# Optimization experiments

Measured on AMD Instinct MI355X. Metric: run time of the kernel, lower is better.

The kernel has to match this reference:

```python
import jax, jax.numpy as jnp
import numpy as np

H = 16
EPS = 1e-6
AUX_COEF = 0.01
TOPK = 2


def _rmsnorm(x, w):
    ms = jnp.mean(x * x, axis=-1, keepdims=True)
    return x * jax.lax.rsqrt(ms + EPS) * w


def _rope(t, cos, sin):
    # t: [B,H,T,hd]; cos/sin: [T, hd//2]
    half = t.shape[-1] // 2
    t1, t2 = t[..., :half], t[..., half:]
    return jnp.concatenate([t1 * cos - t2 * sin, t1 * sin + t2 * cos], axis=-1)


def setup_inputs() -> dict:
    key = jax.random.key(0)
    ks = jax.random.split(key, 16)
    B, T, D = 2, 1024, 1024
    E, I = 8, 4096
    s = lambda k, shp, fan: jax.random.normal(k, shp, dtype=jnp.float32) * (1.0 / np.sqrt(fan))
    return {
        "x": jax.random.normal(ks[0], (B, T, D), dtype=jnp.float32),
        "qkv_w": s(ks[1], (3 * D, D), D),
        "qkv_b": jnp.zeros((3 * D,), jnp.float32),
        "out_w": s(ks[2], (D, D), D),
        "out_b": jnp.zeros((D,), jnp.float32),
        "ln1_w": jnp.ones((D,), jnp.float32),
        "ln2_w": jnp.ones((D,), jnp.float32),
        "gate_w": s(ks[3], (E, D), D),
        "ew1": s(ks[4], (E, I, D), D),
        "eb1": jnp.zeros((E, I), jnp.float32),
        "ew2": s(ks[5], (E, D, I), I),
        "eb2": jnp.zeros((E, D), jnp.float32),
        "ew3": s(ks[6], (E, I, D), D),
        "eb3": jnp.zeros((E, I), jnp.float32),
    }


def _attention(x, qkv_w, qkv_b, out_w, out_b):
    B, T, D = x.shape
    hd = D // H
    half = hd // 2
    qkv = (x @ qkv_w.T + qkv_b).reshape(B, T, H, 3, hd)
    q = jnp.transpose(qkv[..., 0, :], (0, 2, 1, 3))  # [B,H,T,hd]
    k = jnp.transpose(qkv[..., 1, :], (0, 2, 1, 3))
    v = jnp.transpose(qkv[..., 2, :], (0, 2, 1, 3))
    theta = 1.0 / (10000.0 ** (jnp.arange(half, dtype=jnp.float32) / half))
    freq = jnp.arange(T, dtype=jnp.float32)[:, None] * theta[None, :]  # [T,half]
    cos, sin = jnp.cos(freq), jnp.sin(freq)
    q = _rope(q, cos, sin)
    k = _rope(k, cos, sin)
    # NOTE: original scales by embed_dim**-0.5 (not head_dim**-0.5)
    scale = D ** (-0.5)
    scores = jnp.einsum("bhqd,bhkd->bhqk", q, k) * scale
    mask = jnp.triu(jnp.full((T, T), -1e9, dtype=scores.dtype), k=1)
    w = jax.nn.softmax(scores + mask, axis=-1)
    attn = jnp.einsum("bhqk,bhkd->bhqd", w, v)
    attn = jnp.transpose(attn, (0, 2, 1, 3)).reshape(B, T, D)
    return attn @ out_w.T + out_b


def _moe(x, gate_w, ew1, eb1, ew2, eb2, ew3, eb3):
    B, T, D = x.shape
    E = gate_w.shape[0]
    xf = x.reshape(-1, D)  # [N,D]
    N = xf.shape[0]
    probs = jax.nn.softmax(xf @ gate_w.T, axis=-1)  # [N,E]
    topk_vals, topk_idx = jax.lax.top_k(probs, TOPK)
    oh = jax.nn.one_hot(topk_idx, E, dtype=xf.dtype)  # [N,K,E]
    gates = jnp.sum(oh * topk_vals[..., None], axis=1)  # [N,E] dense gate, zero off top-k
    # per-expert SwiGLU over all tokens, combined with sparse gates
    h = jax.nn.silu(jnp.einsum("nd,eid->nei", xf, ew1) + eb1) * (
        jnp.einsum("nd,eid->nei", xf, ew3) + eb3
    )  # [N,E,I]
    out_e = jnp.einsum("nei,edi->ned", h, ew2) + eb2  # [N,E,D]
    y = jnp.einsum("ned,ne->nd", out_e, gates)
    counts = jnp.sum(oh, axis=(0, 1))  # bincount of routed assignments
    f = counts / (N * TOPK)
    P = jnp.mean(probs, axis=0)
    aux = AUX_COEF * E * jnp.dot(f, P)
    return y.reshape(B, T, D), aux


def reference(x, qkv_w, qkv_b, out_w, out_b, ln1_w, ln2_w, gate_w, ew1, eb1, ew2, eb2, ew3, eb3):
    h1 = x + _attention(_rmsnorm(x, ln1_w), qkv_w, qkv_b, out_w, out_b)
    y, aux = _moe(_rmsnorm(h1, ln2_w), gate_w, ew1, eb1, ew2, eb2, ew3, eb3)
    return h1 + y, aux
```

## Files before the change

kernel.cpp:

```cpp
#include <hip/hip_runtime.h>
#include <cstdint>
#include <cstddef>
#include <math.h>

#define T_SEQ  1024
#define DMODEL 1024
#define NHEAD  16
#define HDIM   64
#define NEXP   8
#define IDIM   4096
#define NTOK   2048
#define NSLOT  4096

typedef short bf16x8 __attribute__((ext_vector_type(8)));
typedef short s16x4  __attribute__((ext_vector_type(4)));
typedef float floatx4 __attribute__((ext_vector_type(4)));
typedef unsigned int uintx4 __attribute__((ext_vector_type(4)));

__device__ __forceinline__ float bf2f(short s) {
  return __uint_as_float(((unsigned)(unsigned short)s) << 16);
}
__device__ __forceinline__ short f2bf(float f) {
  unsigned u = __float_as_uint(f);
  unsigned r = (u + 0x7FFFu + ((u >> 16) & 1u)) >> 16;
  return (short)r;
}
__device__ __forceinline__ unsigned cvt_pk_bf16(float lo, float hi) {
  unsigned r;
  asm("v_cvt_pk_bf16_f32 %0, %1, %2" : "=v"(r) : "v"(lo), "v"(hi));
  return r;
}
__device__ __forceinline__ uintx4 pack8_bf16(floatx4 a, floatx4 b) {
  uintx4 u;
  u[0] = cvt_pk_bf16(a[0], a[1]);
  u[1] = cvt_pk_bf16(a[2], a[3]);
  u[2] = cvt_pk_bf16(b[0], b[1]);
  u[3] = cvt_pk_bf16(b[2], b[3]);
  return u;
}
__device__ __forceinline__ void split8(const float* x, uintx4& hi, uintx4& lo) {
  #pragma unroll
  for (int i = 0; i < 4; i++) {
    unsigned h = cvt_pk_bf16(x[2*i], x[2*i+1]);
    hi[i] = h;
    float r0 = x[2*i]   - __uint_as_float(h << 16);
    float r1 = x[2*i+1] - __uint_as_float(h & 0xffff0000u);
    lo[i] = cvt_pk_bf16(r0, r1);
  }
}

__global__ __launch_bounds__(256) void rmsnorm_f32_kernel(
    const float* __restrict__ x, const float* __restrict__ w, float* __restrict__ out) {
  int row = blockIdx.x, tid = threadIdx.x;
  const floatx4* xr = (const floatx4*)(x + (size_t)row * DMODEL);
  floatx4 v = xr[tid];
  float ss = v[0]*v[0] + v[1]*v[1] + v[2]*v[2] + v[3]*v[3];
  #pragma unroll
  for (int off = 32; off > 0; off >>= 1) ss += __shfl_xor(ss, off);
  __shared__ float wsum[4];
  int wid = tid >> 6;
  if ((tid & 63) == 0) wsum[wid] = ss;
  __syncthreads();
  float tot = wsum[0] + wsum[1] + wsum[2] + wsum[3];
  float r = rsqrtf(tot * (1.0f / DMODEL) + 1e-6f);
  floatx4 wv = ((const floatx4*)w)[tid];
  floatx4 o;
  o[0] = v[0]*r*wv[0]; o[1] = v[1]*r*wv[1];
  o[2] = v[2]*r*wv[2]; o[3] = v[3]*r*wv[3];
  ((floatx4*)(out + (size_t)row * DMODEL))[tid] = o;
}

__global__ __launch_bounds__(256) void rmsnorm_bf16_kernel(
    const float* __restrict__ x, const float* __restrict__ w, short* __restrict__ out) {
  int row = blockIdx.x, tid = threadIdx.x;
  const floatx4* xr = (const floatx4*)(x + (size_t)row * DMODEL);
  floatx4 v = xr[tid];
  float ss = v[0]*v[0] + v[1]*v[1] + v[2]*v[2] + v[3]*v[3];
  #pragma unroll
  for (int off = 32; off > 0; off >>= 1) ss += __shfl_xor(ss, off);
  __shared__ float wsum[4];
  int wid = tid >> 6;
  if ((tid & 63) == 0) wsum[wid] = ss;
  __syncthreads();
  float tot = wsum[0] + wsum[1] + wsum[2] + wsum[3];
  float r = rsqrtf(tot * (1.0f / DMODEL) + 1e-6f);
  floatx4 wv = ((const floatx4*)w)[tid];
  s16x4 o;
  o[0] = f2bf(v[0]*r*wv[0]); o[1] = f2bf(v[1]*r*wv[1]);
  o[2] = f2bf(v[2]*r*wv[2]); o[3] = f2bf(v[3]*r*wv[3]);
  *(s16x4*)(out + (size_t)row * DMODEL + tid*4) = o;
}

template<int RESID>
__global__ __launch_bounds__(256) void gemm_3bf16(
    const float* __restrict__ A, const float* __restrict__ W,
    const float* __restrict__ bias, const float* __restrict__ resid,
    float* __restrict__ C, int N, int K) {
  __shared__ __attribute__((aligned(16))) short Ahi[64*40];
  __shared__ __attribute__((aligned(16))) short Alo[64*40];
  __shared__ __attribute__((aligned(16))) short Whi[64*40];
  __shared__ __attribute__((aligned(16))) short Wlo[64*40];
  int tid = threadIdx.x, lane = tid & 63, wid = tid >> 6;
  int wm = wid >> 1, wn = wid & 1;
  int m0 = blockIdx.y * 64, n0 = blockIdx.x * 64;
  floatx4 zero4 = {0.f,0.f,0.f,0.f};
  floatx4 acc[2][2];
  #pragma unroll
  for (int mi = 0; mi < 2; mi++)
    #pragma unroll
    for (int nj = 0; nj < 2; nj++) acc[mi][nj] = zero4;

  int ar = tid >> 2, ak = (tid & 3) * 8;
  const float* Ap = A + (size_t)(m0 + ar) * K + ak;
  const float* Wp = W + (size_t)(n0 + ar) * K + ak;
  int rsel = lane & 15, kseg = (lane >> 4) * 8;

  for (int kk = 0; kk < K; kk += 32) {
    float abuf[8], wbuf[8];
    *(floatx4*)(abuf)     = *(const floatx4*)(Ap + kk);
    *(floatx4*)(abuf + 4) = *(const floatx4*)(Ap + kk + 4);
    *(floatx4*)(wbuf)     = *(const floatx4*)(Wp + kk);
    *(floatx4*)(wbuf + 4) = *(const floatx4*)(Wp + kk + 4);
    uintx4 ahi, alo, whi, wlo;
    split8(abuf, ahi, alo);
    split8(wbuf, whi, wlo);
    __syncthreads();
    *(uintx4*)(&Ahi[ar*40 + ak]) = ahi;
    *(uintx4*)(&Alo[ar*40 + ak]) = alo;
    *(uintx4*)(&Whi[ar*40 + ak]) = whi;
    *(uintx4*)(&Wlo[ar*40 + ak]) = wlo;
    __syncthreads();
    bf16x8 afh[2], afl[2], wfh[2], wfl[2];
    #pragma unroll
    for (int mi = 0; mi < 2; mi++) {
      int row = (wm*32 + mi*16 + rsel)*40 + kseg;
      afh[mi] = *(const bf16x8*)(&Ahi[row]);
      afl[mi] = *(const bf16x8*)(&Alo[row]);
    }
    #pragma unroll
    for (int nj = 0; nj < 2; nj++) {
      int row = (wn*32 + nj*16 + rsel)*40 + kseg;
      wfh[nj] = *(const bf16x8*)(&Whi[row]);
      wfl[nj] = *(const bf16x8*)(&Wlo[row]);
    }
    #pragma unroll
    for (int mi = 0; mi < 2; mi++)
      #pragma unroll
      for (int nj = 0; nj < 2; nj++) {
        acc[mi][nj] = __builtin_amdgcn_mfma_f32_16x16x32_bf16(afl[mi], wfh[nj], acc[mi][nj], 0, 0, 0);
        acc[mi][nj] = __builtin_amdgcn_mfma_f32_16x16x32_bf16(afh[mi], wfl[nj], acc[mi][nj], 0, 0, 0);
        acc[mi][nj] = __builtin_amdgcn_mfma_f32_16x16x32_bf16(afh[mi], wfh[nj], acc[mi][nj], 0, 0, 0);
      }
  }
  int rj = (lane >> 4) * 4, cn = lane & 15;
  #pragma unroll
  for (int mi = 0; mi < 2; mi++) {
    #pragma unroll
    for (int nj = 0; nj < 2; nj++) {
      int n = n0 + wn*32 + nj*16 + cn;
      float bn = bias[n];
      #pragma unroll
      for (int j = 0; j < 4; j++) {
        int m = m0 + wm*32 + mi*16 + rj + j;
        float v = acc[mi][nj][j] + bn;
        if (RESID) v += resid[(size_t)m * N + n];
        C[(size_t)m * N + n] = v;
      }
    }
  }
}

__global__ void rope_table_kernel(float* __restrict__ cost, float* __restrict__ sint) {
  int t = blockIdx.x, d = threadIdx.x;
  double theta = pow(10000.0, -(double)d / 32.0);
  double f = (double)t * theta;
  cost[t*32 + d] = (float)cos(f);
  sint[t*32 + d] = (float)sin(f);
}

__global__ __launch_bounds__(256) void rope_kernel(
    const float* __restrict__ qkv, const float* __restrict__ cost, const float* __restrict__ sint,
    float* __restrict__ qr, float* __restrict__ kr) {
  int wid = threadIdx.x >> 6, lane = threadIdx.x & 63;
  int idx = blockIdx.x * 4 + wid;
  int h = idx & 15, n = idx >> 4;
  int t = n & (T_SEQ - 1), b = n >> 10;
  const float* base = qkv + (size_t)n * 3072 + h * 192;
  int d2 = lane & 31;
  float c = cost[t*32 + d2], s = sint[t*32 + d2];
  float q1 = base[d2],      q2 = base[d2 + 32];
  float k1 = base[64 + d2], k2 = base[96 + d2];
  float qo = (lane < 32) ? (q1*c - q2*s) : (q1*s + q2*c);
  float ko = (lane < 32) ? (k1*c - k2*s) : (k1*s + k2*c);
  size_t orow = ((size_t)(b*NHEAD + h) * T_SEQ + t) * HDIM;
  qr[orow + lane] = qo;
  kr[orow + lane] = ko;
}

__global__ __launch_bounds__(256) void vtrans_kernel(
    const float* __restrict__ qkvf, float* __restrict__ vrT) {
  __shared__ __attribute__((aligned(16))) float tile[64][68];
  int bh = blockIdx.x, t0 = blockIdx.y * 64;
  int b = bh >> 4, h = bh & 15;
  int tid = threadIdx.x;
  int r = tid >> 2, seg = (tid & 3) * 16;
  const float* src = qkvf + ((size_t)(b*T_SEQ + t0 + r))*3072 + h*192 + 128 + seg;
  floatx4 v0 = *(const floatx4*)(src);
  floatx4 v1 = *(const floatx4*)(src + 4);
  floatx4 v2 = *(const floatx4*)(src + 8);
  floatx4 v3 = *(const floatx4*)(src + 12);
  *(floatx4*)(&tile[r][seg])      = v0;
  *(floatx4*)(&tile[r][seg + 4])  = v1;
  *(floatx4*)(&tile[r][seg + 8])  = v2;
  *(floatx4*)(&tile[r][seg + 12]) = v3;
  __syncthreads();
  int dr = r, tseg = seg;
  floatx4 o0, o1, o2, o3;
  #pragma unroll
  for (int i = 0; i < 4; i++) {
    o0[i] = tile[tseg + i][dr];
    o1[i] = tile[tseg + 4 + i][dr];
    o2[i] = tile[tseg + 8 + i][dr];
    o3[i] = tile[tseg + 12 + i][dr];
  }
  float* dst = vrT + ((size_t)(bh*HDIM + dr))*T_SEQ + t0 + tseg;
  *(floatx4*)(dst)      = o0;
  *(floatx4*)(dst + 4)  = o1;
  *(floatx4*)(dst + 8)  = o2;
  *(floatx4*)(dst + 12) = o3;
}

__global__ __launch_bounds__(256) void attn_mfma_kernel(
    const float* __restrict__ qr_, const float* __restrict__ kr_,
    const float* __restrict__ vrT_, float* __restrict__ attno) {
  __shared__ __attribute__((aligned(16))) short Qhi[64*72];
  __shared__ __attribute__((aligned(16))) short Qlo[64*72];
  __shared__ __attribute__((aligned(16))) short Khi[64*72];
  __shared__ __attribute__((aligned(16))) short Klo[64*72];
  __shared__ __attribute__((aligned(16))) short Vhi[64*72];
  __shared__ __attribute__((aligned(16))) short Vlo[64*72];
  __shared__ __attribute__((aligned(16))) unsigned Pp[64*68];
  int tid = threadIdx.x, lane = tid & 63, w = tid >> 6;
  int bh = blockIdx.x;
  int qt = 15 - (int)blockIdx.y;
  int q0 = qt * 64;
  int b = bh >> 4, h = bh & 15;
  const float* Qb  = qr_  + ((size_t)bh * T_SEQ + q0) * HDIM;
  const float* Kb  = kr_  + (size_t)bh * T_SEQ * HDIM;
  const float* Vtb = vrT_ + (size_t)bh * HDIM * T_SEQ;

  int srow = tid >> 2, sseg = (tid & 3) * 16;
  {
    const float* src = Qb + srow*HDIM + sseg;
    float b0[8], b1[8];
    *(floatx4*)(b0)   = *(const floatx4*)(src);
    *(floatx4*)(b0+4) = *(const floatx4*)(src + 4);
    *(floatx4*)(b1)   = *(const floatx4*)(src + 8);
    *(floatx4*)(b1+4) = *(const floatx4*)(src + 12);
    uintx4 h0, l0, h1, l1;
    split8(b0, h0, l0); split8(b1, h1, l1);
    *(uintx4*)(&Qhi[srow*72 + sseg])     = h0;
    *(uintx4*)(&Qhi[srow*72 + sseg + 8]) = h1;
    *(uintx4*)(&Qlo[srow*72 + sseg])     = l0;
    *(uintx4*)(&Qlo[srow*72 + sseg + 8]) = l1;
  }

  int rsel = lane & 15, kseg = (lane >> 4) * 8, cl = lane & 15;
  int rbase = w*16 + (lane >> 4) * 4;
  const float scale = 0.03125f;
  float mrow[4] = {-1e30f,-1e30f,-1e30f,-1e30f};
  float lrow[4] = {0.f,0.f,0.f,0.f};
  floatx4 zero4 = {0.f,0.f,0.f,0.f};
  floatx4 Of[4];
  #pragma unroll
  for (int f = 0; f < 4; f++) Of[f] = zero4;

  int ntiles = qt + 1;
  for (int kt = 0; kt < ntiles; kt++) {
    int kbase = kt << 6;
    const float* kp = Kb  + (size_t)(kbase + srow)*HDIM + sseg;
    const float* vp = Vtb + (size_t)srow*T_SEQ + kbase + sseg;
    float kb0[8], kb1[8], vb0[8], vb1[8];
    *(floatx4*)(kb0)   = *(const floatx4*)(kp);
    *(floatx4*)(kb0+4) = *(const floatx4*)(kp + 4);
    *(floatx4*)(kb1)   = *(const floatx4*)(kp + 8);
    *(floatx4*)(kb1+4) = *(const floatx4*)(kp + 12);
    *(floatx4*)(vb0)   = *(const floatx4*)(vp);
    *(floatx4*)(vb0+4) = *(const floatx4*)(vp + 4);
    *(floatx4*)(vb1)   = *(const floatx4*)(vp + 8);
    *(floatx4*)(vb1+4) = *(const floatx4*)(vp + 12);
    __syncthreads();
    {
      uintx4 h0, l0, h1, l1;
      split8(kb0, h0, l0); split8(kb1, h1, l1);
      *(uintx4*)(&Khi[srow*72 + sseg])     = h0;
      *(uintx4*)(&Khi[srow*72 + sseg + 8]) = h1;
      *(uintx4*)(&Klo[srow*72 + sseg])     = l0;
      *(uintx4*)(&Klo[srow*72 + sseg + 8]) = l1;
      split8(vb0, h0, l0); split8(vb1, h1, l1);
      *(uintx4*)(&Vhi[srow*72 + sseg])     = h0;
      *(uintx4*)(&Vhi[srow*72 + sseg + 8]) = h1;
      *(uintx4*)(&Vlo[srow*72 + sseg])     = l0;
      *(uintx4*)(&Vlo[srow*72 + sseg + 8]) = l1;
    }
    __syncthreads();
    floatx4 sf[4];
    #pragma unroll
    for (int f = 0; f < 4; f++) sf[f] = zero4;
    #pragma unroll
    for (int c = 0; c < 2; c++) {
      int ko = c*32 + kseg;
      bf16x8 qh = *(const bf16x8*)(&Qhi[(w*16 + rsel)*72 + ko]);
      bf16x8 ql = *(const bf16x8*)(&Qlo[(w*16 + rsel)*72 + ko]);
      #pragma unroll
      for (int f = 0; f < 4; f++) {
        bf16x8 kh = *(const bf16x8*)(&Khi[(f*16 + rsel)*72 + ko]);
        bf16x8 kl = *(const bf16x8*)(&Klo[(f*16 + rsel)*72 + ko]);
        sf[f] = __builtin_amdgcn_mfma_f32_16x16x32_bf16(ql, kh, sf[f], 0, 0, 0);
        sf[f] = __builtin_amdgcn_mfma_f32_16x16x32_bf16(qh, kl, sf[f], 0, 0, 0);
        sf[f] = __builtin_amdgcn_mfma_f32_16x16x32_bf16(qh, kh, sf[f], 0, 0, 0);
      }
    }
    float pm[4] = {-1e30f,-1e30f,-1e30f,-1e30f};
    #pragma unroll
    for (int f = 0; f < 4; f++) {
      int col = kbase + f*16 + cl;
      #pragma unroll
      for (int j = 0; j < 4; j++) {
        float s = sf[f][j];
        s = (col <= q0 + rbase + j) ? s*scale : -1e30f;
        sf[f][j] = s;
        pm[j] = fmaxf(pm[j], s);
      }
    }
    #pragma unroll
    for (int off = 1; off < 16; off <<= 1)
      #pragma unroll
      for (int j = 0; j < 4; j++) pm[j] = fmaxf(pm[j], __shfl_xor(pm[j], off));
    float sc[4], rs[4] = {0.f,0.f,0.f,0.f};
    #pragma unroll
    for (int j = 0; j < 4; j++) {
      float mn = fmaxf(mrow[j], pm[j]);
      sc[j] = __expf(mrow[j] - mn);
      mrow[j] = mn;
    }
    #pragma unroll
    for (int f = 0; f < 4; f++) {
      #pragma unroll
      for (int j = 0; j < 4; j++) {
        float p = (sf[f][j] > -1e29f) ? __expf(sf[f][j] - mrow[j]) : 0.f;
        rs[j] += p;
        unsigned hp = cvt_pk_bf16(p, 0.f);
        float ph = __uint_as_float(hp << 16);
        unsigned lp = cvt_pk_bf16(p - ph, 0.f);
        Pp[(rbase + j)*68 + f*16 + cl] = (hp << 16) | (lp & 0xffffu);
      }
    }
    #pragma unroll
    for (int off = 1; off < 16; off <<= 1)
      #pragma unroll
      for (int j = 0; j < 4; j++) rs[j] += __shfl_xor(rs[j], off);
    #pragma unroll
    for (int j = 0; j < 4; j++) lrow[j] = lrow[j]*sc[j] + rs[j];
    #pragma unroll
    for (int f = 0; f < 4; f++)
      #pragma unroll
      for (int j = 0; j < 4; j++) Of[f][j] *= sc[j];
    __syncthreads();
    #pragma unroll
    for (int c = 0; c < 2; c++) {
      int prow = (w*16 + rsel)*68 + c*32 + kseg;
      uintx4 d0 = *(const uintx4*)(&Pp[prow]);
      uintx4 d1 = *(const uintx4*)(&Pp[prow + 4]);
      uintx4 phw, plw;
      phw[0] = (d0[0] >> 16) | (d0[1] & 0xffff0000u);
      phw[1] = (d0[2] >> 16) | (d0[3] & 0xffff0000u);
      phw[2] = (d1[0] >> 16) | (d1[1] & 0xffff0000u);
      phw[3] = (d1[2] >> 16) | (d1[3] & 0xffff0000u);
      plw[0] = (d0[0] & 0xffffu) | (d0[1] << 16);
      plw[1] = (d0[2] & 0xffffu) | (d0[3] << 16);
      plw[2] = (d1[0] & 0xffffu) | (d1[1] << 16);
      plw[3] = (d1[2] & 0xffffu) | (d1[3] << 16);
      bf16x8 Ph = *(bf16x8*)&phw;
      bf16x8 Pl = *(bf16x8*)&plw;
      int ko = c*32 + kseg;
      #pragma unroll
      for (int f = 0; f < 4; f++) {
        bf16x8 vh = *(const bf16x8*)(&Vhi[(f*16 + rsel)*72 + ko]);
        bf16x8 vl = *(const bf16x8*)(&Vlo[(f*16 + rsel)*72 + ko]);
        Of[f] = __builtin_amdgcn_mfma_f32_16x16x32_bf16(Pl, vh, Of[f], 0, 0, 0);
        Of[f] = __builtin_amdgcn_mfma_f32_16x16x32_bf16(Ph, vl, Of[f], 0, 0, 0);
        Of[f] = __builtin_amdgcn_mfma_f32_16x16x32_bf16(Ph, vh, Of[f], 0, 0, 0);
      }
    }
  }
  #pragma unroll
  for (int j = 0; j < 4; j++) {
    float inv = 1.0f / lrow[j];
    size_t rowoff = ((size_t)(b*T_SEQ + q0 + rbase + j))*DMODEL + h*HDIM;
    #pragma unroll
    for (int f = 0; f < 4; f++)
      attno[rowoff + f*16 + cl] = Of[f][j] * inv;
  }
}

__global__ __launch_bounds__(64) void gate_kernel(
    const float* __restrict__ h1, const float* __restrict__ lnw, const float* __restrict__ gw,
    float* __restrict__ probs, int* __restrict__ pair, float* __restrict__ gpair,
    int* __restrict__ counts) {
  int n = blockIdx.x, lane = threadIdx.x;
  const float* xp = h1 + (size_t)n * DMODEL + lane*16;
  float xv[16];
  double ss = 0.0;
  #pragma unroll
  for (int j = 0; j < 16; j++) { xv[j] = xp[j]; ss += (double)xv[j] * (double)xv[j]; }
  #pragma unroll
  for (int off = 32; off > 0; off >>= 1) ss += __shfl_xor(ss, off);
  double r = 1.0 / sqrt(ss * (1.0 / DMODEL) + 1e-6);
  const float* wp = lnw + lane*16;
  double xf[16];
  #pragma unroll
  for (int j = 0; j < 16; j++) xf[j] = (double)xv[j] * r * (double)wp[j];
  double logit[8];
  #pragma unroll
  for (int e = 0; e < 8; e++) {
    const float* g = gw + e*DMODEL + lane*16;
    double acc = 0.0;
    #pragma unroll
    for (int j = 0; j < 16; j++) acc += xf[j] * (double)g[j];
    logit[e] = acc;
  }
  #pragma unroll
  for (int e = 0; e < 8; e++)
    #pragma unroll
    for (int off = 32; off > 0; off >>= 1) logit[e] += __shfl_xor(logit[e], off);
  double mxl = logit[0];
  #pragma unroll
  for (int e = 1; e < 8; e++) mxl = fmax(mxl, logit[e]);
  double p[8], Z = 0.0;
  #pragma unroll
  for (int e = 0; e < 8; e++) { p[e] = exp(logit[e] - mxl); Z += p[e]; }
  double invZ = 1.0 / Z;
  #pragma unroll
  for (int e = 0; e < 8; e++) p[e] *= invZ;
  int e0 = 0; double b0 = p[0];
  #pragma unroll
  for (int e = 1; e < 8; e++) if (p[e] > b0) { b0 = p[e]; e0 = e; }
  int e1 = -1; double b1 = -1.0;
  #pragma unroll
  for (int e = 0; e < 8; e++) if (e != e0 && p[e] > b1) { b1 = p[e]; e1 = e; }
  if (lane == 0) {
    #pragma unroll
    for (int e = 0; e < 8; e++) probs[n*8 + e] = (float)p[e];
    pair[2*n] = e0; pair[2*n+1] = e1;
    gpair[2*n] = (float)b0; gpair[2*n+1] = (float)b1;
    atomicAdd(&counts[e0], 1);
    atomicAdd(&counts[e1], 1);
  }
}

__global__ void offsets_kernel(const int* __restrict__ counts, int* __restrict__ off,
                               int* __restrict__ cursor) {
  if (threadIdx.x == 0) {
    int a = 0;
    for (int e = 0; e < 8; e++) { off[e] = a; cursor[e] = a; a += counts[e]; }
    off[8] = a;
  }
}

__global__ __launch_bounds__(256) void scatter_kernel(
    const int* __restrict__ pair, const float* __restrict__ gpair, int* __restrict__ cursor,
    int* __restrict__ tok_of_slot, float* __restrict__ gate_of_slot, int* __restrict__ slot_of_tok) {
  int n = blockIdx.x * 256 + threadIdx.x;
  int e0 = pair[2*n], e1 = pair[2*n+1];
  int s0 = atomicAdd(&cursor[e0], 1);
  tok_of_slot[s0] = n; gate_of_slot[s0] = gpair[2*n];   slot_of_tok[2*n] = s0;
  int s1 = atomicAdd(&cursor[e1], 1);
  tok_of_slot[s1] = n; gate_of_slot[s1] = gpair[2*n+1]; slot_of_tok[2*n+1] = s1;
}

__global__ __launch_bounds__(256) void aux_kernel(
    const float* __restrict__ probs, const int* __restrict__ counts, float* __restrict__ outaux) {
  __shared__ double sm[256];
  int t = threadIdx.x;
  int e = t & 7, base = t >> 3;
  double acc = 0.0;
  for (int n = base; n < NTOK; n += 32) acc += (double)probs[n*8 + e];
  sm[t] = acc;
  __syncthreads();
  if (t < 8) {
    double s = 0.0;
    for (int g = 0; g < 32; g++) s += sm[g*8 + t];
    sm[t] = s;
  }
  __syncthreads();
  if (t == 0) {
    double aux = 0.0;
    for (int ee = 0; ee < 8; ee++)
      aux += ((double)counts[ee] * (1.0 / (NTOK*2))) * (sm[ee] * (1.0 / NTOK));
    outaux[0] = (float)(0.08 * aux);
  }
}

__global__ __launch_bounds__(256) void moe13_kernel(
    const short* __restrict__ xn2,
    const float* __restrict__ ew1, const float* __restrict__ eb1,
    const float* __restrict__ ew3, const float* __restrict__ eb3,
    const int* __restrict__ counts, const int* __restrict__ off,
    const int* __restrict__ tok_of_slot, short* __restrict__ hbuf) {
  int e = blockIdx.z;
  int Me = counts[e];
  int m0 = blockIdx.y * 128;
  if (m0 >= Me) return;
  int base = off[e];
  int i0 = blockIdx.x * 64;
  __shared__ __attribute__((aligned(16))) short As[128*40];
  __shared__ __attribute__((aligned(16))) short W1s[64*40];
  __shared__ __attribute__((aligned(16))) short W3s[64*40];
  int tid = threadIdx.x, lane = tid & 63, wid = tid >> 6;
  int wm = wid >> 1, wn = wid & 1;
  floatx4 zero4 = {0.f,0.f,0.f,0.f};
  floatx4 acc1[4][2], acc3[4][2];
  #pragma unroll
  for (int mi = 0; mi < 4; mi++)
    #pragma unroll
    for (int nj = 0; nj < 2; nj++) { acc1[mi][nj] = zero4; acc3[mi][nj] = zero4; }

  int ar = tid >> 1, ak = (tid & 1) * 8;
  int am = m0 + ar;
  bool aval = (am < Me);
  const short* Ag = xn2 + (size_t)(aval ? tok_of_slot[base + am] : 0) * DMODEL;
  int wr = tid >> 2, wk = (tid & 3) * 8;
  const float* W1g = ew1 + ((size_t)e*IDIM + i0 + wr)*DMODEL + wk;
  const float* W3g = ew3 + ((size_t)e*IDIM + i0 + wr)*DMODEL + wk;
  int rsel = lane & 15, kseg = (lane >> 4) * 8;

  for (int kk = 0; kk < DMODEL; kk += 32) {
    bf16x8 a0 = {0,0,0,0,0,0,0,0}, a1 = {0,0,0,0,0,0,0,0};
    if (aval) {
      a0 = *(const bf16x8*)(Ag + kk + ak);
      a1 = *(const bf16x8*)(Ag + kk + ak + 16);
    }
    floatx4 u0 = *(const floatx4*)(W1g + kk);
    floatx4 u1 = *(const floatx4*)(W1g + kk + 4);
    floatx4 v0 = *(const floatx4*)(W3g + kk);
    floatx4 v1 = *(const floatx4*)(W3g + kk + 4);
    __syncthreads();
    *(bf16x8*)(&As[ar*40 + ak])      = a0;
    *(bf16x8*)(&As[ar*40 + ak + 16]) = a1;
    *(uintx4*)(&W1s[wr*40 + wk]) = pack8_bf16(u0, u1);
    *(uintx4*)(&W3s[wr*40 + wk]) = pack8_bf16(v0, v1);
    __syncthreads();
    bf16x8 af[4], w1f[2], w3f[2];
    #pragma unroll
    for (int mi = 0; mi < 4; mi++)
      af[mi] = *(const bf16x8*)(&As[(wm*64 + mi*16 + rsel)*40 + kseg]);
    #pragma unroll
    for (int nj = 0; nj < 2; nj++) {
      w1f[nj] = *(const bf16x8*)(&W1s[(wn*32 + nj*16 + rsel)*40 + kseg]);
      w3f[nj] = *(const bf16x8*)(&W3s[(wn*32 + nj*16 + rsel)*40 + kseg]);
    }
    #pragma unroll
    for (int mi = 0; mi < 4; mi++)
      #pragma unroll
      for (int nj = 0; nj < 2; nj++) {
        acc1[mi][nj] = __builtin_amdgcn_mfma_f32_16x16x32_bf16(af[mi], w1f[nj], acc1[mi][nj], 0, 0, 0);
        acc3[mi][nj] = __builtin_amdgcn_mfma_f32_16x16x32_bf16(af[mi], w3f[nj], acc3[mi][nj], 0, 0, 0);
      }
  }
  int rj = (lane >> 4) * 4, cn = lane & 15;
  #pragma unroll
  for (int mi = 0; mi < 4; mi++) {
    #pragma unroll
    for (int nj = 0; nj < 2; nj++) {
      int i = i0 + wn*32 + nj*16 + cn;
      float be1 = eb1[e*IDIM + i], be3 = eb3[e*IDIM + i];
      #pragma unroll
      for (int j = 0; j < 4; j++) {
        int m = m0 + wm*64 + mi*16 + rj + j;
        if (m < Me) {
          float a = acc1[mi][nj][j] + be1;
          float b = acc3[mi][nj][j] + be3;
          float hval = (a / (1.f + __expf(-a))) * b;
          hbuf[(size_t)(base + m)*IDIM + i] = f2bf(hval);
        }
      }
    }
  }
}

__global__ __launch_bounds__(256) void moe2_kernel(
    const short* __restrict__ hbuf, const float* __restrict__ ew2, const float* __restrict__ eb2,
    const int* __restrict__ counts, const int* __restrict__ off,
    const float* __restrict__ gate_of_slot,
    float* __restrict__ y0, float* __restrict__ y1) {
  int e = blockIdx.z;
  int Me = counts[e];
  int m0 = blockIdx.y * 128;
  if (m0 >= Me) return;
  int base = off[e];
  int n0 = (blockIdx.x & 7) * 128;
  int khalf = blockIdx.x >> 3;
  int kbeg = khalf * (IDIM/2);
  __shared__ __attribute__((aligned(16))) short As[128*40];
  __shared__ __attribute__((aligned(16))) short Ws[128*40];
  int tid = threadIdx.x, lane = tid & 63, wid = tid >> 6;
  int wm = wid >> 1, wn = wid & 1;
  floatx4 zero4 = {0.f,0.f,0.f,0.f};
  floatx4 acc[4][4];
  #pragma unroll
  for (int mi = 0; mi < 4; mi++)
    #pragma unroll
    for (int nj = 0; nj < 4; nj++) acc[mi][nj] = zero4;

  int ar = tid >> 1, ak = (tid & 1) * 8, kw = (tid & 1) * 16;
  bool aval = (m0 + ar) < Me;
  const short* Ag = hbuf + (size_t)(base + (aval ? (m0 + ar) : 0)) * IDIM + kbeg;
  const float* Wg = ew2 + ((size_t)e*DMODEL + n0 + ar)*IDIM + kbeg;
  int rsel = lane & 15, kseg = (lane >> 4) * 8;

  for (int kk = 0; kk < IDIM/2; kk += 32) {
    bf16x8 a0 = {0,0,0,0,0,0,0,0}, a1 = {0,0,0,0,0,0,0,0};
    if (aval) {
      a0 = *(const bf16x8*)(Ag + kk + ak);
      a1 = *(const bf16x8*)(Ag + kk + ak + 16);
    }
    floatx4 w0 = *(const floatx4*)(Wg + kk + kw);
    floatx4 w1 = *(const floatx4*)(Wg + kk + kw + 4);
    floatx4 w2 = *(const floatx4*)(Wg + kk + kw + 8);
    floatx4 w3 = *(const floatx4*)(Wg + kk + kw + 12);
    __syncthreads();
    *(bf16x8*)(&As[ar*40 + ak])      = a0;
    *(bf16x8*)(&As[ar*40 + ak + 16]) = a1;
    *(uintx4*)(&Ws[ar*40 + kw])     = pack8_bf16(w0, w1);
    *(uintx4*)(&Ws[ar*40 + kw + 8]) = pack8_bf16(w2, w3);
    __syncthreads();
    bf16x8 af[4], wf[4];
    #pragma unroll
    for (int mi = 0; mi < 4; mi++)
      af[mi] = *(const bf16x8*)(&As[(wm*64 + mi*16 + rsel)*40 + kseg]);
    #pragma unroll
    for (int nj = 0; nj < 4; nj++)
      wf[nj] = *(const bf16x8*)(&Ws[(wn*64 + nj*16 + rsel)*40 + kseg]);
    #pragma unroll
    for (int mi = 0; mi < 4; mi++)
      #pragma unroll
      for (int nj = 0; nj < 4; nj++)
        acc[mi][nj] = __builtin_amdgcn_mfma_f32_16x16x32_bf16(af[mi], wf[nj], acc[mi][nj], 0, 0, 0);
  }
  int rj = (lane >> 4) * 4, cn = lane & 15;
  float* yout = khalf ? y1 : y0;
  #pragma unroll
  for (int mi = 0; mi < 4; mi++) {
    #pragma unroll
    for (int nj = 0; nj < 4; nj++) {
      int n = n0 + wn*64 + nj*16 + cn;
      float bn = khalf ? 0.f : eb2[e*DMODEL + n];
      #pragma unroll
      for (int j = 0; j < 4; j++) {
        int m = m0 + wm*64 + mi*16 + rj + j;
        if (m < Me) {
          float g = gate_of_slot[base + m];
          yout[(size_t)(base + m)*DMODEL + n] = (acc[mi][nj][j] + bn) * g;
        }
      }
    }
  }
}

__global__ __launch_bounds__(256) void combine_kernel(
    const float* __restrict__ h1, const float* __restrict__ y0, const float* __restrict__ y1,
    const int* __restrict__ slot_of_tok, float* __restrict__ out) {
  int n = blockIdx.x, t = threadIdx.x;
  int sA = slot_of_tok[2*n], sB = slot_of_tok[2*n+1];
  const floatx4* a   = (const floatx4*)(h1 + (size_t)n*DMODEL);
  const floatx4* y0a = (const floatx4*)(y0 + (size_t)sA*DMODEL);
  const floatx4* y1a = (const floatx4*)(y1 + (size_t)sA*DMODEL);
  const floatx4* y0b = (const floatx4*)(y0 + (size_t)sB*DMODEL);
  const floatx4* y1b = (const floatx4*)(y1 + (size_t)sB*DMODEL);
  floatx4 v = a[t] + (y0a[t] + y1a[t]) + (y0b[t] + y1b[t]);
  ((floatx4*)(out + (size_t)n*DMODEL))[t] = v;
}

extern "C" void kernel_launch(void* const* d_in, const int* in_sizes, int n_in,
                              void* d_out, int out_size, void* d_ws, size_t ws_size,
                              hipStream_t stream) {
  const float* x      = (const float*)d_in[0];
  const float* qkv_w  = (const float*)d_in[1];
  const float* qkv_b  = (const float*)d_in[2];
  const float* out_w  = (const float*)d_in[3];
  const float* out_b  = (const float*)d_in[4];
  const float* ln1_w  = (const float*)d_in[5];
  const float* ln2_w  = (const float*)d_in[6];
  const float* gate_w = (const float*)d_in[7];
  const float* ew1    = (const float*)d_in[8];
  const float* eb1    = (const float*)d_in[9];
  const float* ew2    = (const float*)d_in[10];
  const float* eb2    = (const float*)d_in[11];
  const float* ew3    = (const float*)d_in[12];
  const float* eb3    = (const float*)d_in[13];
  float* out = (float*)d_out;

  char* ws = (char*)d_ws;
  float* xn1f   = (float*)(ws + 0);
  float* attnof = (float*)(ws + 0);
  float* qkvf   = (float*)(ws + 8388608);
  float* h1     = (float*)(ws + 8388608);
  short* xn2    = (short*)(ws + 16777216);
  float* yslot1 = (float*)(ws + 16777216);
  float* qrf    = (float*)(ws + 33554432);
  float* krf    = (float*)(ws + 41943040);
  float* vrT    = (float*)(ws + 50331648);
  short* hbuf   = (short*)(ws + 33554432);
  float* yslot0 = (float*)(ws + 67108864);
  float* cost         = (float*)(ws + 83886080);
  float* sint         = (float*)(ws + 84017152);
  float* probs        = (float*)(ws + 84148224);
  int*   ctrl         = (int*)  (ws + 84213760);
  int*   pair         = (int*)  (ws + 84214784);
  float* gpair        = (float*)(ws + 84231168);
  int*   slot_of_tok  = (int*)  (ws + 84247552);
  int*   tok_of_slot  = (int*)  (ws + 84263936);
  float* gate_of_slot = (float*)(ws + 84280320);

  int* counts = ctrl;
  int* off    = ctrl + 8;
  int* cursor = ctrl + 20;

  hipMemsetAsync(ctrl, 0, 1024, stream);
  rope_table_kernel<<<T_SEQ, 32, 0, stream>>>(cost, sint);
  rmsnorm_f32_kernel<<<NTOK, 256, 0, stream>>>(x, ln1_w, xn1f);
  gemm_3bf16<0><<<dim3(48, 32), 256, 0, stream>>>(xn1f, qkv_w, qkv_b, nullptr, qkvf, 3072, DMODEL);
  rope_kernel<<<8192, 256, 0, stream>>>(qkvf, cost, sint, qrf, krf);
  vtrans_kernel<<<dim3(32, 16), 256, 0, stream>>>(qkvf, vrT);
  attn_mfma_kernel<<<dim3(32, 16), 256, 0, stream>>>(qrf, krf, vrT, attnof);
  gemm_3bf16<1><<<dim3(16, 32), 256, 0, stream>>>(attnof, out_w, out_b, x, h1, DMODEL, DMODEL);
  rmsnorm_bf16_kernel<<<NTOK, 256, 0, stream>>>(h1, ln2_w, xn2);
  gate_kernel<<<NTOK, 64, 0, stream>>>(h1, ln2_w, gate_w, probs, pair, gpair, counts);
  offsets_kernel<<<1, 64, 0, stream>>>(counts, off, cursor);
  scatter_kernel<<<8, 256, 0, stream>>>(pair, gpair, cursor, tok_of_slot, gate_of_slot, slot_of_tok);
  aux_kernel<<<1, 256, 0, stream>>>(probs, counts, out + 2097152);
  moe13_kernel<<<dim3(64, 16, 8), 256, 0, stream>>>(xn2, ew1, eb1, ew3, eb3, counts, off, tok_of_slot, hbuf);
  moe2_kernel<<<dim3(16, 16, 8), 256, 0, stream>>>(hbuf, ew2, eb2, counts, off, gate_of_slot, yslot0, yslot1);
  combine_kernel<<<NTOK, 256, 0, stream>>>(h1, yslot0, yslot1, slot_of_tok, out);
}
```

Before: 545.2 us.

## Load MoE GEMM operands directly from global memory, dropping LDS staging

```diff
diff --git a/kernel.cpp b/kernel.cpp
--- a/kernel.cpp
+++ b/kernel.cpp
@@ -514,11 +514,10 @@
   if (m0 >= Me) return;
   int base = off[e];
   int i0 = blockIdx.x * 64;
-  __shared__ __attribute__((aligned(16))) short As[128*40];
-  __shared__ __attribute__((aligned(16))) short W1s[64*40];
-  __shared__ __attribute__((aligned(16))) short W3s[64*40];
   int tid = threadIdx.x, lane = tid & 63, wid = tid >> 6;
   int wm = wid >> 1, wn = wid & 1;
+  int rsel = lane & 15, kseg = (lane >> 4) * 8;
+
   floatx4 zero4 = {0.f,0.f,0.f,0.f};
   floatx4 acc1[4][2], acc3[4][2];
   #pragma unroll
@@ -526,39 +525,37 @@
     #pragma unroll
     for (int nj = 0; nj < 2; nj++) { acc1[mi][nj] = zero4; acc3[mi][nj] = zero4; }
 
-  int ar = tid >> 1, ak = (tid & 1) * 8;
-  int am = m0 + ar;
-  bool aval = (am < Me);
-  const short* Ag = xn2 + (size_t)(aval ? tok_of_slot[base + am] : 0) * DMODEL;
-  int wr = tid >> 2, wk = (tid & 3) * 8;
-  const float* W1g = ew1 + ((size_t)e*IDIM + i0 + wr)*DMODEL + wk;
-  const float* W3g = ew3 + ((size_t)e*IDIM + i0 + wr)*DMODEL + wk;
-  int rsel = lane & 15, kseg = (lane >> 4) * 8;
+  const short* aptr[4];
+  #pragma unroll
+  for (int mi = 0; mi < 4; mi++) {
+    int m = m0 + wm*64 + mi*16 + rsel;
+    int tok = (m < Me) ? tok_of_slot[base + m] : 0;
+    aptr[mi] = xn2 + (size_t)tok * DMODEL + kseg;
+  }
+  const float* w1p[2];
+  const float* w3p[2];
+  #pragma unroll
+  for (int nj = 0; nj < 2; nj++) {
+    int i = i0 + wn*32 + nj*16 + rsel;
+    w1p[nj] = ew1 + ((size_t)e*IDIM + i)*DMODEL + kseg;
+    w3p[nj] = ew3 + ((size_t)e*IDIM + i)*DMODEL + kseg;
+  }
 
   for (int kk = 0; kk < DMODEL; kk += 32) {
-    bf16x8 a0 = {0,0,0,0,0,0,0,0}, a1 = {0,0,0,0,0,0,0,0};
-    if (aval) {
-      a0 = *(const bf16x8*)(Ag + kk + ak);
-      a1 = *(const bf16x8*)(Ag + kk + ak + 16);
-    }
-    floatx4 u0 = *(const floatx4*)(W1g + kk);
-    floatx4 u1 = *(const floatx4*)(W1g + kk + 4);
-    floatx4 v0 = *(const floatx4*)(W3g + kk);
-    floatx4 v1 = *(const floatx4*)(W3g + kk + 4);
-    __syncthreads();
-    *(bf16x8*)(&As[ar*40 + ak])      = a0;
-    *(bf16x8*)(&As[ar*40 + ak + 16]) = a1;
-    *(uintx4*)(&W1s[wr*40 + wk]) = pack8_bf16(u0, u1);
-    *(uintx4*)(&W3s[wr*40 + wk]) = pack8_bf16(v0, v1);
-    __syncthreads();
     bf16x8 af[4], w1f[2], w3f[2];
     #pragma unroll
     for (int mi = 0; mi < 4; mi++)
-      af[mi] = *(const bf16x8*)(&As[(wm*64 + mi*16 + rsel)*40 + kseg]);
+      af[mi] = *(const bf16x8*)(aptr[mi] + kk);
     #pragma unroll
     for (int nj = 0; nj < 2; nj++) {
-      w1f[nj] = *(const bf16x8*)(&W1s[(wn*32 + nj*16 + rsel)*40 + kseg]);
-      w3f[nj] = *(const bf16x8*)(&W3s[(wn*32 + nj*16 + rsel)*40 + kseg]);
+      floatx4 u0 = *(const floatx4*)(w1p[nj] + kk);
+      floatx4 u1 = *(const floatx4*)(w1p[nj] + kk + 4);
+      uintx4 pw = pack8_bf16(u0, u1);
+      w1f[nj] = *(bf16x8*)&pw;
+      floatx4 v0 = *(const floatx4*)(w3p[nj] + kk);
+      floatx4 v1 = *(const floatx4*)(w3p[nj] + kk + 4);
+      uintx4 pv = pack8_bf16(v0, v1);
+      w3f[nj] = *(bf16x8*)&pv;
     }
     #pragma unroll
     for (int mi = 0; mi < 4; mi++)
@@ -602,10 +599,10 @@
   int n0 = (blockIdx.x & 7) * 128;
   int khalf = blockIdx.x >> 3;
   int kbeg = khalf * (IDIM/2);
-  __shared__ __attribute__((aligned(16))) short As[128*40];
-  __shared__ __attribute__((aligned(16))) short Ws[128*40];
   int tid = threadIdx.x, lane = tid & 63, wid = tid >> 6;
   int wm = wid >> 1, wn = wid & 1;
+  int rsel = lane & 15, kseg = (lane >> 4) * 8;
+
   floatx4 zero4 = {0.f,0.f,0.f,0.f};
   floatx4 acc[4][4];
   #pragma unroll
@@ -613,35 +610,32 @@
     #pragma unroll
     for (int nj = 0; nj < 4; nj++) acc[mi][nj] = zero4;
 
-  int ar = tid >> 1, ak = (tid & 1) * 8, kw = (tid & 1) * 16;
-  bool aval = (m0 + ar) < Me;
-  const short* Ag = hbuf + (size_t)(base + (aval ? (m0 + ar) : 0)) * IDIM + kbeg;
-  const float* Wg = ew2 + ((size_t)e*DMODEL + n0 + ar)*IDIM + kbeg;
-  int rsel = lane & 15, kseg = (lane >> 4) * 8;
+  const short* aptr[4];
+  #pragma unroll
+  for (int mi = 0; mi < 4; mi++) {
+    int m = m0 + wm*64 + mi*16 + rsel;
+    int row = base + ((m < Me) ? m : 0);
+    aptr[mi] = hbuf + (size_t)row*IDIM + kbeg + kseg;
+  }
+  const float* wp[4];
+  #pragma unroll
+  for (int nj = 0; nj < 4; nj++) {
+    int n = n0 + wn*64 + nj*16 + rsel;
+    wp[nj] = ew2 + ((size_t)e*DMODEL + n)*IDIM + kbeg + kseg;
+  }
 
   for (int kk = 0; kk < IDIM/2; kk += 32) {
-    bf16x8 a0 = {0,0,0,0,0,0,0,0}, a1 = {0,0,0,0,0,0,0,0};
-    if (aval) {
-      a0 = *(const bf16x8*)(Ag + kk + ak);
-      a1 = *(const bf16x8*)(Ag + kk + ak + 16);
-    }
-    floatx4 w0 = *(const floatx4*)(Wg + kk + kw);
-    floatx4 w1 = *(const floatx4*)(Wg + kk + kw + 4);
-    floatx4 w2 = *(const floatx4*)(Wg + kk + kw + 8);
-    floatx4 w3 = *(const floatx4*)(Wg + kk + kw + 12);
-    __syncthreads();
-    *(bf16x8*)(&As[ar*40 + ak])      = a0;
-    *(bf16x8*)(&As[ar*40 + ak + 16]) = a1;
-    *(uintx4*)(&Ws[ar*40 + kw])     = pack8_bf16(w0, w1);
-    *(uintx4*)(&Ws[ar*40 + kw + 8]) = pack8_bf16(w2, w3);
-    __syncthreads();
     bf16x8 af[4], wf[4];
     #pragma unroll
     for (int mi = 0; mi < 4; mi++)
-      af[mi] = *(const bf16x8*)(&As[(wm*64 + mi*16 + rsel)*40 + kseg]);
-    #pragma unroll
-    for (int nj = 0; nj < 4; nj++)
-      wf[nj] = *(const bf16x8*)(&Ws[(wn*64 + nj*16 + rsel)*40 + kseg]);
+      af[mi] = *(const bf16x8*)(aptr[mi] + kk);
+    #pragma unroll
+    for (int nj = 0; nj < 4; nj++) {
+      floatx4 u0 = *(const floatx4*)(wp[nj] + kk);
+      floatx4 u1 = *(const floatx4*)(wp[nj] + kk + 4);
+      uintx4 pw = pack8_bf16(u0, u1);
+      wf[nj] = *(bf16x8*)&pw;
+    }
     #pragma unroll
     for (int mi = 0; mi < 4; mi++)
       #pragma unroll
@@ -660,8 +654,8 @@
       for (int j = 0; j < 4; j++) {
         int m = m0 + wm*64 + mi*16 + rj + j;
         if (m < Me) {
-          float g = gate_of_slot[base + m];
-          yout[(size_t)(base + m)*DMODEL + n] = (acc[mi][nj][j] + bn) * g;
+          float gv = gate_of_slot[base + m];
+          yout[(size_t)(base + m)*DMODEL + n] = (acc[mi][nj][j] + bn) * gv;
         }
       }
     }
```

Result: slower. 938.9 us (+72.2%).

## Double-buffer shared memory tiles in MoE gate/up GEMM kernel

Applied to the files above, without the earlier changes.

```diff
diff --git a/kernel.cpp b/kernel.cpp
--- a/kernel.cpp
+++ b/kernel.cpp
@@ -514,9 +514,9 @@
   if (m0 >= Me) return;
   int base = off[e];
   int i0 = blockIdx.x * 64;
-  __shared__ __attribute__((aligned(16))) short As[128*40];
-  __shared__ __attribute__((aligned(16))) short W1s[64*40];
-  __shared__ __attribute__((aligned(16))) short W3s[64*40];
+  __shared__ __attribute__((aligned(16))) short As[2][128*40];
+  __shared__ __attribute__((aligned(16))) short W1s[2][64*40];
+  __shared__ __attribute__((aligned(16))) short W3s[2][64*40];
   int tid = threadIdx.x, lane = tid & 63, wid = tid >> 6;
   int wm = wid >> 1, wn = wid & 1;
   floatx4 zero4 = {0.f,0.f,0.f,0.f};
@@ -535,30 +535,47 @@
   const float* W3g = ew3 + ((size_t)e*IDIM + i0 + wr)*DMODEL + wk;
   int rsel = lane & 15, kseg = (lane >> 4) * 8;
 
-  for (int kk = 0; kk < DMODEL; kk += 32) {
+  {
     bf16x8 a0 = {0,0,0,0,0,0,0,0}, a1 = {0,0,0,0,0,0,0,0};
     if (aval) {
-      a0 = *(const bf16x8*)(Ag + kk + ak);
-      a1 = *(const bf16x8*)(Ag + kk + ak + 16);
-    }
-    floatx4 u0 = *(const floatx4*)(W1g + kk);
-    floatx4 u1 = *(const floatx4*)(W1g + kk + 4);
-    floatx4 v0 = *(const floatx4*)(W3g + kk);
-    floatx4 v1 = *(const floatx4*)(W3g + kk + 4);
-    __syncthreads();
-    *(bf16x8*)(&As[ar*40 + ak])      = a0;
-    *(bf16x8*)(&As[ar*40 + ak + 16]) = a1;
-    *(uintx4*)(&W1s[wr*40 + wk]) = pack8_bf16(u0, u1);
-    *(uintx4*)(&W3s[wr*40 + wk]) = pack8_bf16(v0, v1);
-    __syncthreads();
+      a0 = *(const bf16x8*)(Ag + ak);
+      a1 = *(const bf16x8*)(Ag + ak + 16);
+    }
+    floatx4 u0 = *(const floatx4*)(W1g);
+    floatx4 u1 = *(const floatx4*)(W1g + 4);
+    floatx4 v0 = *(const floatx4*)(W3g);
+    floatx4 v1 = *(const floatx4*)(W3g + 4);
+    *(bf16x8*)(&As[0][ar*40 + ak])      = a0;
+    *(bf16x8*)(&As[0][ar*40 + ak + 16]) = a1;
+    *(uintx4*)(&W1s[0][wr*40 + wk]) = pack8_bf16(u0, u1);
+    *(uintx4*)(&W3s[0][wr*40 + wk]) = pack8_bf16(v0, v1);
+  }
+  __syncthreads();
+
+  for (int kk = 0; kk < DMODEL; kk += 32) {
+    int cur = (kk >> 5) & 1;
+    int nxt = cur ^ 1;
+    bool more = (kk + 32 < DMODEL);
+    bf16x8 na0 = {0,0,0,0,0,0,0,0}, na1 = {0,0,0,0,0,0,0,0};
+    floatx4 nu0, nu1, nv0, nv1;
+    if (more) {
+      if (aval) {
+        na0 = *(const bf16x8*)(Ag + kk + 32 + ak);
+        na1 = *(const bf16x8*)(Ag + kk + 32 + ak + 16);
+      }
+      nu0 = *(const floatx4*)(W1g + kk + 32);
+      nu1 = *(const floatx4*)(W1g + kk + 36);
+      nv0 = *(const floatx4*)(W3g + kk + 32);
+      nv1 = *(const floatx4*)(W3g + kk + 36);
+    }
     bf16x8 af[4], w1f[2], w3f[2];
     #pragma unroll
     for (int mi = 0; mi < 4; mi++)
-      af[mi] = *(const bf16x8*)(&As[(wm*64 + mi*16 + rsel)*40 + kseg]);
+      af[mi] = *(const bf16x8*)(&As[cur][(wm*64 + mi*16 + rsel)*40 + kseg]);
     #pragma unroll
     for (int nj = 0; nj < 2; nj++) {
-      w1f[nj] = *(const bf16x8*)(&W1s[(wn*32 + nj*16 + rsel)*40 + kseg]);
-      w3f[nj] = *(const bf16x8*)(&W3s[(wn*32 + nj*16 + rsel)*40 + kseg]);
+      w1f[nj] = *(const bf16x8*)(&W1s[cur][(wn*32 + nj*16 + rsel)*40 + kseg]);
+      w3f[nj] = *(const bf16x8*)(&W3s[cur][(wn*32 + nj*16 + rsel)*40 + kseg]);
     }
     #pragma unroll
     for (int mi = 0; mi < 4; mi++)
@@ -567,6 +584,13 @@
         acc1[mi][nj] = __builtin_amdgcn_mfma_f32_16x16x32_bf16(af[mi], w1f[nj], acc1[mi][nj], 0, 0, 0);
         acc3[mi][nj] = __builtin_amdgcn_mfma_f32_16x16x32_bf16(af[mi], w3f[nj], acc3[mi][nj], 0, 0, 0);
       }
+    if (more) {
+      *(bf16x8*)(&As[nxt][ar*40 + ak])      = na0;
+      *(bf16x8*)(&As[nxt][ar*40 + ak + 16]) = na1;
+      *(uintx4*)(&W1s[nxt][wr*40 + wk]) = pack8_bf16(nu0, nu1);
+      *(uintx4*)(&W3s[nxt][wr*40 + wk]) = pack8_bf16(nv0, nv1);
+    }
+    __syncthreads();
   }
   int rj = (lane >> 4) * 4, cn = lane & 15;
   #pragma unroll
```

New measurement: 539.3 us. No clear change (-1.1%).
